# Kernel optimization log

Hardware: AMD Instinct MI355X
Metric: run time of the kernel (lower is better)

## Reference

```python
import jax, jax.numpy as jnp
import numpy as np

N, IN_DIM, HID, M, T, E, A, OUT = 10000, 256, 256, 8, 3, 160000, 2000, 10
LN_EPS = 1e-5


def _layernorm(x, g, b):
    mu = x.mean(-1, keepdims=True)
    var = ((x - mu) ** 2).mean(-1, keepdims=True)
    return (x - mu) * jax.lax.rsqrt(var + LN_EPS) * g + b


def _gcn_conv(x, w, b, src, dst, n):
    # PyG GCNConv: x' = D^{-1/2}(A+I)D^{-1/2} (x W) + b, deg counted on dst with self-loops
    xw = x @ w  # [n, out]
    loops = jnp.arange(n, dtype=src.dtype)
    s = jnp.concatenate([src, loops])
    d = jnp.concatenate([dst, loops])
    deg = jax.ops.segment_sum(jnp.ones(d.shape[0], xw.dtype), d, num_segments=n)
    dinv = jax.lax.rsqrt(jnp.maximum(deg, 1.0))
    norm = dinv[s] * dinv[d]
    out = jax.ops.segment_sum(xw[s] * norm[:, None], d, num_segments=n)
    return out + b


def setup_inputs() -> dict:
    key = jax.random.key(0)
    ks = jax.random.split(key, 26)
    g = lambda i, shape: (jax.random.normal(ks[i], shape, jnp.float32) * 0.02)
    return {
        "edge_index_t": jax.random.randint(ks[0], (T, 2, E), 0, N),
        "node_t": jax.random.randint(ks[1], (T, A), 0, N),
        "m": M,
        "emb": g(2, (N, IN_DIM)),
        "gcn_w1": g(3, (IN_DIM, HID)), "gcn_b1": jnp.zeros((HID,), jnp.float32),
        "gcn_w2": g(4, (HID, HID)), "gcn_b2": jnp.zeros((HID,), jnp.float32),
        "ln1_g": jnp.ones((HID,), jnp.float32), "ln1_b": jnp.zeros((HID,), jnp.float32),
        "tok_w1": g(5, (M, M)), "tok_b1": jnp.zeros((M,), jnp.float32),
        "tok_w2": g(6, (M, M)), "tok_b2": jnp.zeros((M,), jnp.float32),
        "ln2_g": jnp.ones((HID,), jnp.float32), "ln2_b": jnp.zeros((HID,), jnp.float32),
        "ch_w1": g(7, (HID, HID)), "ch_b1": jnp.zeros((HID,), jnp.float32),
        "ch_w2": g(8, (HID, HID)), "ch_b2": jnp.zeros((HID,), jnp.float32),
        "pred_w": g(9, (HID, HID)), "pred_b": jnp.zeros((HID,), jnp.float32),
        "cls1_w": g(10, (HID, HID)), "cls1_b": jnp.zeros((HID,), jnp.float32),
        "cls2_w": g(11, (HID, OUT)), "cls2_b": jnp.zeros((OUT,), jnp.float32),
    }


def reference(edge_index_t, node_t, m, emb,
              gcn_w1, gcn_b1, gcn_w2, gcn_b2,
              ln1_g, ln1_b, tok_w1, tok_b1, tok_w2, tok_b2,
              ln2_g, ln2_b, ch_w1, ch_b1, ch_w2, ch_b2,
              pred_w, pred_b, cls1_w, cls1_b, cls2_w, cls2_b):
    n = emb.shape[0]

    def mixer(xm):  # [n, m, hid]
        y = _layernorm(xm, ln1_g, ln1_b)
        # token MLP over the m axis (transpose(1,2) in torch)
        y = jnp.einsum('nmh,mk->nkh', y, tok_w1) + tok_b1[None, :, None]
        y = jax.nn.gelu(y, approximate=False)
        y = jnp.einsum('nmh,mk->nkh', y, tok_w2) + tok_b2[None, :, None]
        x = xm + y
        z = _layernorm(x, ln2_g, ln2_b)
        z = jax.nn.gelu(z @ ch_w1 + ch_b1, approximate=False) @ ch_w2 + ch_b2
        return x + z

    def step(x_m, inp):
        src, dst, nid = inp
        # forecast from current window (before this step's graph update)
        x_new = mixer(x_m).mean(axis=1)  # discrete FinalProcessLayer: mean over tokens
        # 2-layer GCN on the (shared) initial embeddings
        x = _gcn_conv(emb, gcn_w1, gcn_b1, src, dst, n)
        x = jax.nn.relu(x)
        x = _gcn_conv(x, gcn_w2, gcn_b2, src, dst, n)
        # boolean-mask scatter: zero rows of nodes listed in node_t[i]
        x = x.at[nid].set(0.0)
        x_m = jnp.concatenate([x_m[:, 1:, :], x[:, None, :]], axis=1)
        return x_m, x_new

    x_m0 = jnp.zeros((n, m, HID), emb.dtype)
    _, v = jax.lax.scan(step, x_m0, (edge_index_t[:, 0], edge_index_t[:, 1], node_t))
    # InvariantPredictor over all T timesteps at once: v [T, n, hid]
    h = jnp.tanh(v @ pred_w + pred_b)
    y_hat = jax.nn.relu((h @ cls1_w + cls1_b) @ cls2_w + cls2_b)
    return h, y_hat
```

## Files before the change

kernel.cpp:

```cpp
#include <hip/hip_runtime.h>
#include <math.h>

#define NN 10000
#define HIDD 256
#define MTOK 8
#define TT 3
#define EE 160000
#define AA 2000
#define OUTD 10
#define LNEPS 1e-5f

typedef unsigned short u16;
typedef __attribute__((ext_vector_type(8))) __bf16 bf16x8;
typedef __attribute__((ext_vector_type(4))) float f32x4;

__device__ __forceinline__ float gelu_f(float x) {
    return 0.5f * x * (1.f + erff(x * 0.7071067811865475f));
}
__device__ __forceinline__ u16 f2bf(float x) {
    unsigned u = __builtin_bit_cast(unsigned, x);
    return (u16)((u + 0x7FFFu + ((u >> 16) & 1u)) >> 16);
}
__device__ __forceinline__ float bf2f(u16 b) {
    return __builtin_bit_cast(float, (unsigned)b << 16);
}
__device__ __forceinline__ void gload16(const void* g, void* l) {
    __builtin_amdgcn_global_load_lds(
        (const __attribute__((address_space(1))) unsigned int*)g,
        (__attribute__((address_space(3))) unsigned int*)l, 16, 0, 0);
}

__global__ void count_kernel(const int* __restrict__ edge, int* __restrict__ cnt) {
    int g = blockIdx.y;
    const int* dst = edge + (size_t)g * 2 * EE + EE;
    int e = blockIdx.x * 256 + threadIdx.x;
    if (e < EE) atomicAdd(&cnt[g * NN + dst[e]], 1);
}

__global__ __launch_bounds__(1024) void scan_kernel(const int* __restrict__ cnt_all,
        int* __restrict__ rowstart_all, int* __restrict__ cursor_all, float* __restrict__ dinv_all) {
    int g = blockIdx.x;
    const int* cnt = cnt_all + (size_t)g * NN;
    int* rowstart = rowstart_all + (size_t)g * NN;
    int* cursor = cursor_all + (size_t)g * NN;
    float* dinv = dinv_all + (size_t)g * NN;
    __shared__ int wsum[16];
    int tid = threadIdx.x, lane = tid & 63, wid = tid >> 6;
    int carry = 0;
    for (int base = 0; base < NN; base += 1024) {
        int i = base + tid;
        int v = (i < NN) ? cnt[i] : 0;
        int s = v;
        #pragma unroll
        for (int o = 1; o < 64; o <<= 1) {
            int t = __shfl_up(s, o, 64);
            if (lane >= o) s += t;
        }
        if (lane == 63) wsum[wid] = s;
        __syncthreads();
        if (wid == 0) {
            int ws = (lane < 16) ? wsum[lane] : 0;
            #pragma unroll
            for (int o = 1; o < 16; o <<= 1) {
                int t = __shfl_up(ws, o, 64);
                if (lane >= o) ws += t;
            }
            if (lane < 16) wsum[lane] = ws;
        }
        __syncthreads();
        int woff = (wid > 0) ? wsum[wid - 1] : 0;
        int tot = wsum[15];
        if (i < NN) {
            int excl = carry + s + woff - v;
            rowstart[i] = excl;
            cursor[i] = excl;
            dinv[i] = rsqrtf((float)(v + 1));
        }
        carry += tot;
        __syncthreads();
    }
}

__global__ void fill_kernel(const int* __restrict__ edge, int* __restrict__ cursor, int* __restrict__ esrc) {
    int g = blockIdx.y;
    const int* src = edge + (size_t)g * 2 * EE;
    const int* dst = src + EE;
    int e = blockIdx.x * 256 + threadIdx.x;
    if (e < EE) {
        int d = dst[e];
        int idx = atomicAdd(&cursor[g * NN + d], 1);
        esrc[(size_t)g * EE + idx] = src[e];
    }
}

template<int RELU, int WF32, int WSPLIT>
__global__ __launch_bounds__(256) void gcn_agg(const float* __restrict__ xw, size_t xw_goff,
        const int* __restrict__ esrc_all, const int* __restrict__ rowstart_all,
        const int* __restrict__ cnt_all, const float* __restrict__ dinv_all,
        const float* __restrict__ bias, float* __restrict__ out,
        u16* __restrict__ ohi, u16* __restrict__ olo) {
    int g = blockIdx.y;
    const float* xwg = xw + (size_t)g * xw_goff;
    const int* esrc = esrc_all + (size_t)g * EE;
    const int* rowstart = rowstart_all + (size_t)g * NN;
    const int* cntp = cnt_all + (size_t)g * NN;
    const float* dinv = dinv_all + (size_t)g * NN;
    int wave = threadIdx.x >> 6, lane = threadIdx.x & 63;
    int d = blockIdx.x * 4 + wave;
    if (d >= NN) return;
    int start = rowstart[d];
    int len = cntp[d];
    float dd = dinv[d];
    int h = lane * 4;
    float4 a = *(const float4*)&xwg[(size_t)d * HIDD + h];
    float4 acc;
    acc.x = a.x * dd; acc.y = a.y * dd; acc.z = a.z * dd; acc.w = a.w * dd;
    for (int i = 0; i < len; i++) {
        int s = esrc[start + i];
        float ds = dinv[s];
        float4 b = *(const float4*)&xwg[(size_t)s * HIDD + h];
        acc.x = fmaf(b.x, ds, acc.x);
        acc.y = fmaf(b.y, ds, acc.y);
        acc.z = fmaf(b.z, ds, acc.z);
        acc.w = fmaf(b.w, ds, acc.w);
    }
    float o0 = acc.x * dd + bias[h + 0];
    float o1 = acc.y * dd + bias[h + 1];
    float o2 = acc.z * dd + bias[h + 2];
    float o3 = acc.w * dd + bias[h + 3];
    if (RELU) {
        o0 = fmaxf(o0, 0.f); o1 = fmaxf(o1, 0.f); o2 = fmaxf(o2, 0.f); o3 = fmaxf(o3, 0.f);
    }
    size_t obase = (size_t)g * NN * HIDD + (size_t)d * HIDD + h;
    if (WF32) {
        float4 o; o.x = o0; o.y = o1; o.z = o2; o.w = o3;
        *(float4*)&out[obase] = o;
    }
    if (WSPLIT) {
        ushort4 hv, lv;
        u16 h0 = f2bf(o0), h1 = f2bf(o1), h2 = f2bf(o2), h3 = f2bf(o3);
        hv.x = h0; hv.y = h1; hv.z = h2; hv.w = h3;
        lv.x = f2bf(o0 - bf2f(h0)); lv.y = f2bf(o1 - bf2f(h1));
        lv.z = f2bf(o2 - bf2f(h2)); lv.w = f2bf(o3 - bf2f(h3));
        *(ushort4*)&ohi[obase] = hv;
        *(ushort4*)&olo[obase] = lv;
    }
}

__global__ void mask_kernel(const int* __restrict__ node_t, float* __restrict__ xs) {
    int g = blockIdx.y;
    int node = node_t[(size_t)g * AA + blockIdx.x];
    xs[(size_t)g * NN * HIDD + (size_t)node * HIDD + threadIdx.x] = 0.f;
}

__global__ void split_kernel(const float* __restrict__ x, u16* __restrict__ hi, u16* __restrict__ lo, int n) {
    int i = blockIdx.x * 256 + threadIdx.x;
    if (i < n) {
        float v = x[i];
        u16 h = f2bf(v);
        hi[i] = h;
        lo[i] = f2bf(v - bf2f(h));
    }
}

__global__ void wsplit_all(const float* __restrict__ w0, const float* __restrict__ w1,
        const float* __restrict__ w2, const float* __restrict__ w3,
        const float* __restrict__ w4, const float* __restrict__ w5, u16* __restrict__ bt) {
    const float* W[6] = { w0, w1, w2, w3, w4, w5 };
    const float* Wm = W[blockIdx.y];
    u16* Bt = bt + (size_t)blockIdx.y * 256 * 768;
    int c = blockIdx.x, k = threadIdx.x;
    float x = Wm[k * 256 + c];
    u16 hi = f2bf(x), lo = f2bf(x - bf2f(hi));
    Bt[c * 768 + k] = hi;
    Bt[c * 768 + 256 + k] = hi;
    Bt[c * 768 + 512 + k] = lo;
}

template<int ACT, int WF32, int WSPLIT, int EPI>
__global__ __launch_bounds__(256) void gemm_split(
        const u16* __restrict__ Ahi, const u16* __restrict__ Alo,
        const u16* __restrict__ Bt, const float* __restrict__ bias,
        float* __restrict__ outf, u16* __restrict__ ohi, u16* __restrict__ olo,
        const float* __restrict__ xsum, int R) {
    __shared__ __align__(16) u16 ldsA[2][128 * 64];
    __shared__ __align__(16) u16 ldsB[2][128 * 64];
    int tid = threadIdx.x;
    int lane = tid & 63, w = tid >> 6;
    int nwg = gridDim.x, orig = blockIdx.x;
    int xcd = orig & 7, i8 = orig >> 3;
    int q = nwg >> 3, r = nwg & 7;
    int bid = (xcd < r ? xcd * (q + 1) : r * (q + 1) + (xcd - r) * q) + i8;
    int rowbase = (bid >> 1) * 128;
    int cb = bid & 1;
    int wrow = (w >> 1) * 64, wcol = (w & 1) * 64;
    f32x4 acc[4][4];
    #pragma unroll
    for (int i = 0; i < 4; i++)
        #pragma unroll
        for (int j = 0; j < 4; j++) acc[i][j] = f32x4{0.f, 0.f, 0.f, 0.f};

    constexpr int KCH[12]  = {0,4,1,5,2,6,3,7,8,9,10,11};
    constexpr int BNEW[12] = {1,0,1,0,1,0,1,0,1,1,1,1};
    constexpr int BBUF[12] = {0,0,1,1,0,0,1,1,0,1,0,1};

    auto stageA = [&](int buf, int c) {
        const u16* Aseg = (c >= 4 && c < 8) ? Alo : Ahi;
        int koff = (c & 3) * 64;
        #pragma unroll
        for (int i = 0; i < 4; i++) {
            int j = i * 256 + tid;
            int rr = j >> 3, sl = j & 7;
            int grow = rowbase + rr; if (grow > R - 1) grow = R - 1;
            const u16* gp = Aseg + (size_t)grow * 256 + koff + ((sl ^ (rr & 7)) << 3);
            gload16(gp, &ldsA[buf][(i * 256 + (tid & 192)) << 3]);
        }
    };
    auto stageB = [&](int buf, int c) {
        #pragma unroll
        for (int i = 0; i < 4; i++) {
            int j = i * 256 + tid;
            int rr = j >> 3, sl = j & 7;
            const u16* gp = Bt + (size_t)(cb * 128 + rr) * 768 + c * 64 + ((sl ^ (rr & 7)) << 3);
            gload16(gp, &ldsB[buf][(i * 256 + (tid & 192)) << 3]);
        }
    };

    stageA(0, KCH[0]);
    stageB(0, KCH[0]);
    #pragma unroll
    for (int c = 0; c < 12; c++) {
        int cur = c & 1;
        if (c < 11) {
            stageA(cur ^ 1, KCH[c + 1]);
            if (BNEW[c + 1]) {
                stageB(BBUF[c + 1], KCH[c + 1]);
                asm volatile("s_waitcnt vmcnt(8)" ::: "memory");
            } else {
                asm volatile("s_waitcnt vmcnt(4)" ::: "memory");
            }
        } else {
            asm volatile("s_waitcnt vmcnt(0)" ::: "memory");
        }
        __builtin_amdgcn_s_barrier();
        __builtin_amdgcn_sched_barrier(0);
        __builtin_amdgcn_s_setprio(1);
        #pragma unroll
        for (int ks = 0; ks < 2; ks++) {
            bf16x8 a[4], b[4];
            #pragma unroll
            for (int rf = 0; rf < 4; rf++) {
                int rr = wrow + rf * 16 + (lane & 15);
                int slot = (lane >> 4) + ks * 4;
                a[rf] = *(const bf16x8*)&ldsA[cur][(rr << 6) + ((slot ^ (rr & 7)) << 3)];
            }
            #pragma unroll
            for (int cf = 0; cf < 4; cf++) {
                int cc = wcol + cf * 16 + (lane & 15);
                int slot = (lane >> 4) + ks * 4;
                b[cf] = *(const bf16x8*)&ldsB[BBUF[c]][(cc << 6) + ((slot ^ (cc & 7)) << 3)];
            }
            #pragma unroll
            for (int rf = 0; rf < 4; rf++)
                #pragma unroll
                for (int cf = 0; cf < 4; cf++)
                    acc[rf][cf] = __builtin_amdgcn_mfma_f32_16x16x32_bf16(a[rf], b[cf], acc[rf][cf], 0, 0, 0);
        }
        __builtin_amdgcn_s_setprio(0);
        __builtin_amdgcn_sched_barrier(0);
        __builtin_amdgcn_s_barrier();
    }
    #pragma unroll
    for (int rf = 0; rf < 4; rf++) {
        #pragma unroll
        for (int cf = 0; cf < 4; cf++) {
            int col = cb * 128 + wcol + cf * 16 + (lane & 15);
            float bv = bias[col];
            f32x4 v = acc[rf][cf];
            if (EPI == 1) {
                float s = 0.f;
                #pragma unroll
                for (int r2 = 0; r2 < 4; r2++) s += gelu_f(v[r2] + bv);
                float o = __shfl_xor(s, 16, 64);
                float nodesum = s + o;
                if (((lane >> 4) & 1) == 0) {
                    int node = ((rowbase + wrow + rf * 16) >> 3) + ((lane >> 4) >> 1);
                    u16 hi = f2bf(nodesum), lo = f2bf(nodesum - bf2f(hi));
                    ohi[(size_t)node * 256 + col] = hi;
                    olo[(size_t)node * 256 + col] = lo;
                }
            } else if (EPI == 2) {
                int row0 = rowbase + wrow + rf * 16 + ((lane >> 4) << 2);
                #pragma unroll
                for (int r2 = 0; r2 < 4; r2++) {
                    int row = row0 + r2;
                    if (row < R) {
                        float val = (xsum[(size_t)row * 256 + col] + v[r2] + 8.f * bv) * 0.125f;
                        u16 hi = f2bf(val), lo = f2bf(val - bf2f(hi));
                        ohi[(size_t)row * 256 + col] = hi;
                        olo[(size_t)row * 256 + col] = lo;
                    }
                }
            } else {
                int row0 = rowbase + wrow + rf * 16 + ((lane >> 4) << 2);
                #pragma unroll
                for (int r2 = 0; r2 < 4; r2++) {
                    int row = row0 + r2;
                    if (row < R) {
                        float val = v[r2] + bv;
                        if (ACT == 1) val = gelu_f(val);
                        if (ACT == 2) val = tanhf(val);
                        if (WF32) outf[(size_t)row * 256 + col] = val;
                        if (WSPLIT) {
                            u16 hi = f2bf(val), lo = f2bf(val - bf2f(hi));
                            ohi[(size_t)row * 256 + col] = hi;
                            olo[(size_t)row * 256 + col] = lo;
                        }
                    }
                }
            }
        }
    }
}

__global__ __launch_bounds__(256) void mixer_front(
        const float* __restrict__ xs, int nodebase,
        const float* __restrict__ ln1_g, const float* __restrict__ ln1_b,
        const float* __restrict__ tw1, const float* __restrict__ tb1,
        const float* __restrict__ tw2, const float* __restrict__ tb2,
        const float* __restrict__ ln2_g, const float* __restrict__ ln2_b,
        u16* __restrict__ z_hi, u16* __restrict__ z_lo, float* __restrict__ xsum_out) {
    int nv = nodebase + blockIdx.x;
    int step = nv >= NN ? 1 : 0;
    int n = nv - step * NN;
    const float* p1 = xs + ((size_t)step * NN + n) * HIDD;
    const float* p2 = step ? xs + (size_t)n * HIDD : nullptr;
    int tid = threadIdx.x;
    int wave = tid >> 6, lane = tid & 63;
    __shared__ __align__(16) float sx[MTOK][HIDD];
    __shared__ float stw1[64], stw2[64], stb1[8], stb2[8];
    __shared__ float red[MTOK][2];
    if (tid < 64) { stw1[tid] = tw1[tid]; stw2[tid] = tw2[tid]; }
    if (tid < 8)  { stb1[tid] = tb1[tid]; stb2[tid] = tb2[tid]; }
    #pragma unroll
    for (int m = 0; m < MTOK; m++) {
        const float* src = (m == MTOK - 1) ? p1 : (m == MTOK - 2) ? p2 : nullptr;
        sx[m][tid] = src ? src[tid] : 0.f;
    }
    __syncthreads();
    float g1v = ln1_g[tid], b1v = ln1_b[tid];
    #pragma unroll
    for (int rep = 0; rep < 2; rep++) {
        int m = wave + rep * 4;
        float x0 = sx[m][lane], x1 = sx[m][lane + 64], x2 = sx[m][lane + 128], x3 = sx[m][lane + 192];
        float s = x0 + x1 + x2 + x3;
        float ss = x0 * x0 + x1 * x1 + x2 * x2 + x3 * x3;
        for (int off = 32; off > 0; off >>= 1) { s += __shfl_down(s, off, 64); ss += __shfl_down(ss, off, 64); }
        if (lane == 0) {
            float mu = s * (1.f / HIDD);
            float var = ss * (1.f / HIDD) - mu * mu;
            red[m][0] = mu;
            red[m][1] = rsqrtf(var + LNEPS);
        }
    }
    __syncthreads();
    float ty[MTOK];
    #pragma unroll
    for (int m = 0; m < MTOK; m++) ty[m] = (sx[m][tid] - red[m][0]) * red[m][1] * g1v + b1v;
    float u[MTOK];
    #pragma unroll
    for (int k = 0; k < MTOK; k++) {
        float a = stb1[k];
        #pragma unroll
        for (int m = 0; m < MTOK; m++) a = fmaf(ty[m], stw1[m * MTOK + k], a);
        u[k] = gelu_f(a);
    }
    #pragma unroll
    for (int k = 0; k < MTOK; k++) {
        float a = stb2[k];
        #pragma unroll
        for (int m = 0; m < MTOK; m++) a = fmaf(u[m], stw2[m * MTOK + k], a);
        sx[k][tid] += a;
    }
    __syncthreads();
    float xsm = 0.f;
    #pragma unroll
    for (int m = 0; m < MTOK; m++) xsm += sx[m][tid];
    xsum_out[(size_t)nv * HIDD + tid] = xsm;
    float g2v = ln2_g[tid], b2v = ln2_b[tid];
    #pragma unroll
    for (int rep = 0; rep < 2; rep++) {
        int m = wave + rep * 4;
        float x0 = sx[m][lane], x1 = sx[m][lane + 64], x2 = sx[m][lane + 128], x3 = sx[m][lane + 192];
        float s = x0 + x1 + x2 + x3;
        float ss = x0 * x0 + x1 * x1 + x2 * x2 + x3 * x3;
        for (int off = 32; off > 0; off >>= 1) { s += __shfl_down(s, off, 64); ss += __shfl_down(ss, off, 64); }
        if (lane == 0) {
            float mu = s * (1.f / HIDD);
            float var = ss * (1.f / HIDD) - mu * mu;
            red[m][0] = mu;
            red[m][1] = rsqrtf(var + LNEPS);
        }
    }
    __syncthreads();
    #pragma unroll
    for (int m = 0; m < MTOK; m++) {
        float z = (sx[m][tid] - red[m][0]) * red[m][1] * g2v + b2v;
        u16 hi = f2bf(z), lo = f2bf(z - bf2f(hi));
        size_t idx = ((size_t)blockIdx.x * MTOK + m) * HIDD + tid;
        z_hi[idx] = hi;
        z_lo[idx] = lo;
    }
}

__global__ __launch_bounds__(256) void mixer_kernel(
        const float* __restrict__ ln1_g, const float* __restrict__ ln1_b,
        const float* __restrict__ tw1, const float* __restrict__ tb1,
        const float* __restrict__ tw2, const float* __restrict__ tb2,
        const float* __restrict__ ln2_g, const float* __restrict__ ln2_b,
        const float* __restrict__ cw1, const float* __restrict__ cb1,
        const float* __restrict__ cw2, const float* __restrict__ cb2,
        float* __restrict__ vout) {
    int tid = threadIdx.x;
    __shared__ __align__(16) float sx[MTOK][HIDD];
    __shared__ __align__(16) float sy[MTOK][HIDD];
    __shared__ float stw1[64], stw2[64], stb1[8], stb2[8];
    if (tid < 64) { stw1[tid] = tw1[tid]; stw2[tid] = tw2[tid]; }
    if (tid < 8)  { stb1[tid] = tb1[tid]; stb2[tid] = tb2[tid]; }
    __syncthreads();
    float b1v = ln1_b[tid];
    float ty[MTOK];
    #pragma unroll
    for (int m = 0; m < MTOK; m++) ty[m] = b1v;
    float u[MTOK];
    #pragma unroll
    for (int k = 0; k < MTOK; k++) {
        float a = stb1[k];
        #pragma unroll
        for (int m = 0; m < MTOK; m++) a = fmaf(ty[m], stw1[m * MTOK + k], a);
        u[k] = gelu_f(a);
    }
    #pragma unroll
    for (int k = 0; k < MTOK; k++) {
        float a = stb2[k];
        #pragma unroll
        for (int m = 0; m < MTOK; m++) a = fmaf(u[m], stw2[m * MTOK + k], a);
        sx[k][tid] = a;
    }
    __syncthreads();
    __shared__ float red[MTOK][2];
    int wave = tid >> 6, lane = tid & 63;
    float g2v = ln2_g[tid], b2v = ln2_b[tid];
    #pragma unroll
    for (int rep = 0; rep < 2; rep++) {
        int m = wave + rep * 4;
        float x0 = sx[m][lane], x1 = sx[m][lane + 64], x2 = sx[m][lane + 128], x3 = sx[m][lane + 192];
        float s = x0 + x1 + x2 + x3;
        float ss = x0 * x0 + x1 * x1 + x2 * x2 + x3 * x3;
        for (int off = 32; off > 0; off >>= 1) { s += __shfl_down(s, off, 64); ss += __shfl_down(ss, off, 64); }
        if (lane == 0) {
            float mu = s * (1.f / HIDD);
            float var = ss * (1.f / HIDD) - mu * mu;
            red[m][0] = mu;
            red[m][1] = rsqrtf(var + LNEPS);
        }
    }
    __syncthreads();
    #pragma unroll
    for (int m = 0; m < MTOK; m++) sy[m][tid] = (sx[m][tid] - red[m][0]) * red[m][1] * g2v + b2v;
    __syncthreads();
    float acc[MTOK];
    #pragma unroll
    for (int m = 0; m < MTOK; m++) acc[m] = 0.f;
    for (int h = 0; h < HIDD; h += 4) {
        float w0 = cw1[(h + 0) * HIDD + tid];
        float w1 = cw1[(h + 1) * HIDD + tid];
        float w2 = cw1[(h + 2) * HIDD + tid];
        float w3 = cw1[(h + 3) * HIDD + tid];
        #pragma unroll
        for (int m = 0; m < MTOK; m++) {
            const float4 a = *(const float4*)&sy[m][h];
            acc[m] = fmaf(a.x, w0, acc[m]);
            acc[m] = fmaf(a.y, w1, acc[m]);
            acc[m] = fmaf(a.z, w2, acc[m]);
            acc[m] = fmaf(a.w, w3, acc[m]);
        }
    }
    __syncthreads();
    float cb1v = cb1[tid];
    #pragma unroll
    for (int m = 0; m < MTOK; m++) sy[m][tid] = gelu_f(acc[m] + cb1v);
    __syncthreads();
    float acc2[MTOK];
    #pragma unroll
    for (int m = 0; m < MTOK; m++) acc2[m] = 0.f;
    for (int h = 0; h < HIDD; h += 4) {
        float w0 = cw2[(h + 0) * HIDD + tid];
        float w1 = cw2[(h + 1) * HIDD + tid];
        float w2 = cw2[(h + 2) * HIDD + tid];
        float w3 = cw2[(h + 3) * HIDD + tid];
        #pragma unroll
        for (int m = 0; m < MTOK; m++) {
            const float4 a = *(const float4*)&sy[m][h];
            acc2[m] = fmaf(a.x, w0, acc2[m]);
            acc2[m] = fmaf(a.y, w1, acc2[m]);
            acc2[m] = fmaf(a.z, w2, acc2[m]);
            acc2[m] = fmaf(a.w, w3, acc2[m]);
        }
    }
    float cb2v = cb2[tid];
    float ssum = 0.f;
    #pragma unroll
    for (int m = 0; m < MTOK; m++) ssum += sx[m][tid] + acc2[m] + cb2v;
    vout[tid] = ssum * (1.f / MTOK);
}

__global__ __launch_bounds__(256) void t0_head(const float* __restrict__ v0row,
        const float* __restrict__ pred_w, const float* __restrict__ pred_b,
        const float* __restrict__ cls1_w, const float* __restrict__ cls1_b,
        const float* __restrict__ cls2_w, const float* __restrict__ cls2_b,
        float* __restrict__ h0row, float* __restrict__ y0row) {
    __shared__ float s[HIDD], s2[HIDD];
    int tid = threadIdx.x;
    s[tid] = v0row[tid];
    __syncthreads();
    float a = 0.f;
    for (int k = 0; k < HIDD; k++) a = fmaf(s[k], pred_w[k * HIDD + tid], a);
    float h = tanhf(a + pred_b[tid]);
    h0row[tid] = h;
    s2[tid] = h;
    __syncthreads();
    a = 0.f;
    for (int k = 0; k < HIDD; k++) a = fmaf(s2[k], cls1_w[k * HIDD + tid], a);
    float g = a + cls1_b[tid];
    __syncthreads();
    s[tid] = g;
    __syncthreads();
    if (tid < OUTD) {
        float y = 0.f;
        for (int k = 0; k < HIDD; k++) y = fmaf(s[k], cls2_w[k * OUTD + tid], y);
        y0row[tid] = fmaxf(y + cls2_b[tid], 0.f);
    }
}

__global__ void bcast_both(const float* __restrict__ h0row, const float* __restrict__ y0row,
        float* __restrict__ hout, float* __restrict__ yout) {
    int n = blockIdx.x, tid = threadIdx.x;
    hout[(size_t)n * HIDD + tid] = h0row[tid];
    if (tid < OUTD) yout[(size_t)n * OUTD + tid] = y0row[tid];
}

__global__ __launch_bounds__(256) void cls2_kernel(const float* __restrict__ g1, const float* __restrict__ wm,
        const float* __restrict__ b, float* __restrict__ out, int rows) {
    __shared__ float sw[HIDD][12];
    int tid = threadIdx.x;
    for (int i = tid; i < HIDD * OUTD; i += 256) sw[i / OUTD][i % OUTD] = wm[i];
    __syncthreads();
    int rl = tid >> 4, kk = tid & 15;
    int r = blockIdx.x * 16 + rl;
    if (r < rows && kk < OUTD) {
        float acc = 0.f;
        const float* grow = g1 + (size_t)r * HIDD;
        for (int h = 0; h < HIDD; h++) acc = fmaf(grow[h], sw[h][kk], acc);
        out[(size_t)r * OUTD + kk] = fmaxf(acc + b[kk], 0.f);
    }
}

extern "C" void kernel_launch(void* const* d_in, const int* in_sizes, int n_in,
                              void* d_out, int out_size, void* d_ws, size_t ws_size,
                              hipStream_t stream) {
    const int* edge    = (const int*)d_in[0];
    const int* node_t  = (const int*)d_in[1];
    const float* emb   = (const float*)d_in[3];
    const float* gcn_w1 = (const float*)d_in[4];
    const float* gcn_b1 = (const float*)d_in[5];
    const float* gcn_w2 = (const float*)d_in[6];
    const float* gcn_b2 = (const float*)d_in[7];
    const float* ln1_g = (const float*)d_in[8];
    const float* ln1_b = (const float*)d_in[9];
    const float* tw1   = (const float*)d_in[10];
    const float* tb1   = (const float*)d_in[11];
    const float* tw2   = (const float*)d_in[12];
    const float* tb2   = (const float*)d_in[13];
    const float* ln2_g = (const float*)d_in[14];
    const float* ln2_b = (const float*)d_in[15];
    const float* cw1   = (const float*)d_in[16];
    const float* cb1   = (const float*)d_in[17];
    const float* cw2   = (const float*)d_in[18];
    const float* cb2   = (const float*)d_in[19];
    const float* pred_w = (const float*)d_in[20];
    const float* pred_b = (const float*)d_in[21];
    const float* cls1_w = (const float*)d_in[22];
    const float* cls1_b = (const float*)d_in[23];
    const float* cls2_w = (const float*)d_in[24];
    const float* cls2_b = (const float*)d_in[25];

    const size_t NH = (size_t)NN * HIDD;
    char* wsb = (char*)d_ws;
    size_t off = 0;
    auto alloc = [&](size_t bytes) { char* p = wsb + off; off = (off + bytes + 255) & ~(size_t)255; return p; };
    float* xs   = (float*)alloc(2 * NH * 4);
    u16* v_hi   = (u16*)alloc(2 * NH * 2);
    u16* v_lo   = (u16*)alloc(2 * NH * 2);
    u16* h_hi   = (u16*)alloc(2 * NH * 2);
    u16* h_lo   = (u16*)alloc(2 * NH * 2);
    float* xw2  = (float*)alloc(2 * NH * 4);
    float* xsum = (float*)alloc(2 * NH * 4);
    u16* Bt_all = (u16*)alloc((size_t)6 * 256 * 768 * 2);
    u16* Bt_cw1  = Bt_all;
    u16* Bt_cw2  = Bt_all + 1 * 256 * 768;
    u16* Bt_pred = Bt_all + 2 * 256 * 768;
    u16* Bt_cls1 = Bt_all + 3 * 256 * 768;
    u16* Bt_gw1  = Bt_all + 4 * 256 * 768;
    u16* Bt_gw2  = Bt_all + 5 * 256 * 768;
    float* dinv  = (float*)alloc(2 * NN * 4);
    float* zeros = (float*)alloc(HIDD * 4);
    float* v0row = (float*)alloc(HIDD * 4);
    float* h0row = (float*)alloc(HIDD * 4);
    float* y0row = (float*)alloc(16 * 4);
    int* cnt    = (int*)alloc(2 * NN * 4);
    int* rowst  = (int*)alloc(2 * NN * 4);
    int* cursor = (int*)alloc(2 * NN * 4);
    int* esrc   = (int*)alloc((size_t)2 * EE * 4);
    float* xw    = (float*)h_hi;
    u16*  emb_hi = h_lo;
    u16*  emb_lo = h_lo + NH;
    u16*  agg_hi = v_hi;
    u16*  agg_lo = v_lo;
    u16*  s2_hi  = (u16*)xw2;
    u16*  s2_lo  = (u16*)xw2 + 2 * NH;
    float* g1    = xw2;
    size_t remain = (ws_size > off + 4096) ? (ws_size - off - 4096) : 0;
    int CHN = (int)(remain / 8192);
    if (CHN > 2 * NN) CHN = 2 * NN;
    CHN &= ~15;
    if (CHN < 16) CHN = 16;
    const size_t ZE = (size_t)CHN * MTOK * HIDD;
    u16* z_hi  = (u16*)alloc(ZE * 2);
    u16* z_lo  = (u16*)alloc(ZE * 2);

    float* h_out = (float*)d_out;
    float* y_out = h_out + (size_t)TT * NH;

    hipMemsetAsync(zeros, 0, HIDD * sizeof(float), stream);
    wsplit_all<<<dim3(256, 6), 256, 0, stream>>>(cw1, cw2, pred_w, cls1_w, gcn_w1, gcn_w2, Bt_all);
    split_kernel<<<(NN * HIDD + 255) / 256, 256, 0, stream>>>(emb, emb_hi, emb_lo, NN * HIDD);
    gemm_split<0, 1, 0, 0><<<2 * ((NN + 127) / 128), 256, 0, stream>>>(
        emb_hi, emb_lo, Bt_gw1, zeros, xw, nullptr, nullptr, nullptr, NN);

    mixer_kernel<<<1, 256, 0, stream>>>(ln1_g, ln1_b, tw1, tb1, tw2, tb2,
        ln2_g, ln2_b, cw1, cb1, cw2, cb2, v0row);
    t0_head<<<1, 256, 0, stream>>>(v0row, pred_w, pred_b, cls1_w, cls1_b,
        cls2_w, cls2_b, h0row, y0row);
    bcast_both<<<NN, 256, 0, stream>>>(h0row, y0row, h_out, y_out);

    hipMemsetAsync(cnt, 0, 2 * NN * sizeof(int), stream);
    count_kernel<<<dim3((EE + 255) / 256, 2), 256, 0, stream>>>(edge, cnt);
    scan_kernel<<<2, 1024, 0, stream>>>(cnt, rowst, cursor, dinv);
    fill_kernel<<<dim3((EE + 255) / 256, 2), 256, 0, stream>>>(edge, cursor, esrc);
    gcn_agg<1, 0, 1><<<dim3((NN + 3) / 4, 2), 256, 0, stream>>>(xw, 0,
        esrc, rowst, cnt, dinv, gcn_b1, nullptr, agg_hi, agg_lo);
    gemm_split<0, 1, 0, 0><<<2 * ((2 * NN + 127) / 128), 256, 0, stream>>>(
        agg_hi, agg_lo, Bt_gw2, zeros, xw2, nullptr, nullptr, nullptr, 2 * NN);
    gcn_agg<0, 1, 0><<<dim3((NN + 3) / 4, 2), 256, 0, stream>>>(xw2, NH,
        esrc, rowst, cnt, dinv, gcn_b2, xs, nullptr, nullptr);
    mask_kernel<<<dim3(AA, 2), 256, 0, stream>>>(node_t, xs);

    for (int nb = 0; nb < 2 * NN; nb += CHN) {
        int nodes = 2 * NN - nb < CHN ? 2 * NN - nb : CHN;
        int R = nodes * MTOK;
        int rb = (R + 127) / 128;
        mixer_front<<<nodes, 256, 0, stream>>>(xs, nb,
            ln1_g, ln1_b, tw1, tb1, tw2, tb2, ln2_g, ln2_b, z_hi, z_lo, xsum);
        gemm_split<1, 0, 0, 1><<<2 * rb, 256, 0, stream>>>(
            z_hi, z_lo, Bt_cw1, cb1, nullptr,
            s2_hi + (size_t)nb * HIDD, s2_lo + (size_t)nb * HIDD, nullptr, R);
    }
    gemm_split<0, 0, 0, 2><<<2 * ((2 * NN + 127) / 128), 256, 0, stream>>>(
        s2_hi, s2_lo, Bt_cw2, cb2, nullptr, v_hi, v_lo, xsum, 2 * NN);
    gemm_split<2, 1, 1, 0><<<2 * ((2 * NN + 127) / 128), 256, 0, stream>>>(
        v_hi, v_lo, Bt_pred, pred_b,
        h_out + NH, h_hi, h_lo, nullptr, 2 * NN);
    gemm_split<0, 1, 0, 0><<<2 * ((2 * NN + 127) / 128), 256, 0, stream>>>(
        h_hi, h_lo, Bt_cls1, cls1_b, g1, nullptr, nullptr, nullptr, 2 * NN);
    cls2_kernel<<<(2 * NN + 15) / 16, 256, 0, stream>>>(g1, cls2_w, cls2_b, y_out + (size_t)NN * OUTD, 2 * NN);
}
```

Before: 583.9 us.

## Fuse token-mixer front and cw1 GEMM into one kernel keeping z in LDS

Merges the mixer_front kernel (LayerNorms plus the token MLP) with the following cw1 GEMM. Each block now processes 4 nodes (32 rows) and keeps the bf16 hi/lo z tile in shared memory, while streaming the cw1 weight through double-buffered LDS. The chunked global z_hi/z_lo buffer and its write/read round trip disappear, along with the multi-launch loop. In exchange, each block redoes the full B-matrix load for only 32 rows, which raises weight traffic and leaves small, possibly underutilised MFMA tiles.

```diff
diff --git a/kernel.cpp b/kernel.cpp
--- a/kernel.cpp
+++ b/kernel.cpp
@@ -277,19 +277,7 @@
             int col = cb * 128 + wcol + cf * 16 + (lane & 15);
             float bv = bias[col];
             f32x4 v = acc[rf][cf];
-            if (EPI == 1) {
-                float s = 0.f;
-                #pragma unroll
-                for (int r2 = 0; r2 < 4; r2++) s += gelu_f(v[r2] + bv);
-                float o = __shfl_xor(s, 16, 64);
-                float nodesum = s + o;
-                if (((lane >> 4) & 1) == 0) {
-                    int node = ((rowbase + wrow + rf * 16) >> 3) + ((lane >> 4) >> 1);
-                    u16 hi = f2bf(nodesum), lo = f2bf(nodesum - bf2f(hi));
-                    ohi[(size_t)node * 256 + col] = hi;
-                    olo[(size_t)node * 256 + col] = lo;
-                }
-            } else if (EPI == 2) {
+            if (EPI == 2) {
                 int row0 = rowbase + wrow + rf * 16 + ((lane >> 4) << 2);
                 #pragma unroll
                 for (int r2 = 0; r2 < 4; r2++) {
@@ -323,93 +311,182 @@
     }
 }
 
-__global__ __launch_bounds__(256) void mixer_front(
-        const float* __restrict__ xs, int nodebase,
+__global__ __launch_bounds__(256, 2) void mixer_cw1(
+        const float* __restrict__ xs, const u16* __restrict__ Bt, const float* __restrict__ cb1,
         const float* __restrict__ ln1_g, const float* __restrict__ ln1_b,
         const float* __restrict__ tw1, const float* __restrict__ tb1,
         const float* __restrict__ tw2, const float* __restrict__ tb2,
         const float* __restrict__ ln2_g, const float* __restrict__ ln2_b,
-        u16* __restrict__ z_hi, u16* __restrict__ z_lo, float* __restrict__ xsum_out) {
-    int nv = nodebase + blockIdx.x;
-    int step = nv >= NN ? 1 : 0;
-    int n = nv - step * NN;
-    const float* p1 = xs + ((size_t)step * NN + n) * HIDD;
-    const float* p2 = step ? xs + (size_t)n * HIDD : nullptr;
-    int tid = threadIdx.x;
-    int wave = tid >> 6, lane = tid & 63;
+        float* __restrict__ xsum_out, u16* __restrict__ s2_hi, u16* __restrict__ s2_lo) {
     __shared__ __align__(16) float sx[MTOK][HIDD];
+    __shared__ __align__(16) u16 zhi[32 * 256];
+    __shared__ __align__(16) u16 zlo[32 * 256];
+    __shared__ __align__(16) u16 ldsB[2][128 * 64];
     __shared__ float stw1[64], stw2[64], stb1[8], stb2[8];
     __shared__ float red[MTOK][2];
+    int tid = threadIdx.x, lane = tid & 63, w = tid >> 6;
+
+    auto stageB = [&](int buf, int chunk, int ch) {
+        #pragma unroll
+        for (int i = 0; i < 4; i++) {
+            int j = i * 256 + tid;
+            int rr = j >> 3, sl = j & 7;
+            const u16* gp = Bt + (size_t)(ch * 128 + rr) * 768 + chunk * 64 + ((sl ^ (rr & 7)) << 3);
+            gload16(gp, &ldsB[buf][(i * 256 + (tid & 192)) << 3]);
+        }
+    };
+
     if (tid < 64) { stw1[tid] = tw1[tid]; stw2[tid] = tw2[tid]; }
     if (tid < 8)  { stb1[tid] = tb1[tid]; stb2[tid] = tb2[tid]; }
-    #pragma unroll
-    for (int m = 0; m < MTOK; m++) {
-        const float* src = (m == MTOK - 1) ? p1 : (m == MTOK - 2) ? p2 : nullptr;
-        sx[m][tid] = src ? src[tid] : 0.f;
-    }
-    __syncthreads();
+    stageB(0, 0, 0);
+
     float g1v = ln1_g[tid], b1v = ln1_b[tid];
-    #pragma unroll
-    for (int rep = 0; rep < 2; rep++) {
-        int m = wave + rep * 4;
-        float x0 = sx[m][lane], x1 = sx[m][lane + 64], x2 = sx[m][lane + 128], x3 = sx[m][lane + 192];
-        float s = x0 + x1 + x2 + x3;
-        float ss = x0 * x0 + x1 * x1 + x2 * x2 + x3 * x3;
-        for (int off = 32; off > 0; off >>= 1) { s += __shfl_down(s, off, 64); ss += __shfl_down(ss, off, 64); }
-        if (lane == 0) {
-            float mu = s * (1.f / HIDD);
-            float var = ss * (1.f / HIDD) - mu * mu;
-            red[m][0] = mu;
-            red[m][1] = rsqrtf(var + LNEPS);
-        }
-    }
-    __syncthreads();
-    float ty[MTOK];
-    #pragma unroll
-    for (int m = 0; m < MTOK; m++) ty[m] = (sx[m][tid] - red[m][0]) * red[m][1] * g1v + b1v;
-    float u[MTOK];
-    #pragma unroll
-    for (int k = 0; k < MTOK; k++) {
-        float a = stb1[k];
-        #pragma unroll
-        for (int m = 0; m < MTOK; m++) a = fmaf(ty[m], stw1[m * MTOK + k], a);
-        u[k] = gelu_f(a);
-    }
-    #pragma unroll
-    for (int k = 0; k < MTOK; k++) {
-        float a = stb2[k];
-        #pragma unroll
-        for (int m = 0; m < MTOK; m++) a = fmaf(u[m], stw2[m * MTOK + k], a);
-        sx[k][tid] += a;
-    }
-    __syncthreads();
-    float xsm = 0.f;
-    #pragma unroll
-    for (int m = 0; m < MTOK; m++) xsm += sx[m][tid];
-    xsum_out[(size_t)nv * HIDD + tid] = xsm;
     float g2v = ln2_g[tid], b2v = ln2_b[tid];
-    #pragma unroll
-    for (int rep = 0; rep < 2; rep++) {
-        int m = wave + rep * 4;
-        float x0 = sx[m][lane], x1 = sx[m][lane + 64], x2 = sx[m][lane + 128], x3 = sx[m][lane + 192];
-        float s = x0 + x1 + x2 + x3;
-        float ss = x0 * x0 + x1 * x1 + x2 * x2 + x3 * x3;
-        for (int off = 32; off > 0; off >>= 1) { s += __shfl_down(s, off, 64); ss += __shfl_down(ss, off, 64); }
-        if (lane == 0) {
-            float mu = s * (1.f / HIDD);
-            float var = ss * (1.f / HIDD) - mu * mu;
-            red[m][0] = mu;
-            red[m][1] = rsqrtf(var + LNEPS);
-        }
-    }
-    __syncthreads();
-    #pragma unroll
-    for (int m = 0; m < MTOK; m++) {
-        float z = (sx[m][tid] - red[m][0]) * red[m][1] * g2v + b2v;
-        u16 hi = f2bf(z), lo = f2bf(z - bf2f(hi));
-        size_t idx = ((size_t)blockIdx.x * MTOK + m) * HIDD + tid;
-        z_hi[idx] = hi;
-        z_lo[idx] = lo;
+
+    for (int i = 0; i < 4; i++) {
+        int nv = blockIdx.x * 4 + i;
+        int step = nv >= NN ? 1 : 0;
+        int n = nv - step * NN;
+        const float* p1 = xs + ((size_t)step * NN + n) * HIDD;
+        const float* p2 = step ? xs + (size_t)n * HIDD : nullptr;
+        __syncthreads();
+        #pragma unroll
+        for (int m = 0; m < MTOK; m++) {
+            const float* src = (m == MTOK - 1) ? p1 : (m == MTOK - 2) ? p2 : nullptr;
+            sx[m][tid] = src ? src[tid] : 0.f;
+        }
+        __syncthreads();
+        #pragma unroll
+        for (int rep = 0; rep < 2; rep++) {
+            int m = w + rep * 4;
+            float x0 = sx[m][lane], x1 = sx[m][lane + 64], x2 = sx[m][lane + 128], x3 = sx[m][lane + 192];
+            float s = x0 + x1 + x2 + x3;
+            float ss = x0 * x0 + x1 * x1 + x2 * x2 + x3 * x3;
+            for (int off = 32; off > 0; off >>= 1) { s += __shfl_down(s, off, 64); ss += __shfl_down(ss, off, 64); }
+            if (lane == 0) {
+                float mu = s * (1.f / HIDD);
+                float var = ss * (1.f / HIDD) - mu * mu;
+                red[m][0] = mu;
+                red[m][1] = rsqrtf(var + LNEPS);
+            }
+        }
+        __syncthreads();
+        float ty[MTOK];
+        #pragma unroll
+        for (int m = 0; m < MTOK; m++) ty[m] = (sx[m][tid] - red[m][0]) * red[m][1] * g1v + b1v;
+        float u[MTOK];
+        #pragma unroll
+        for (int k = 0; k < MTOK; k++) {
+            float a = stb1[k];
+            #pragma unroll
+            for (int m = 0; m < MTOK; m++) a = fmaf(ty[m], stw1[m * MTOK + k], a);
+            u[k] = gelu_f(a);
+        }
+        #pragma unroll
+        for (int k = 0; k < MTOK; k++) {
+            float a = stb2[k];
+            #pragma unroll
+            for (int m = 0; m < MTOK; m++) a = fmaf(u[m], stw2[m * MTOK + k], a);
+            sx[k][tid] += a;
+        }
+        __syncthreads();
+        float xsm = 0.f;
+        #pragma unroll
+        for (int m = 0; m < MTOK; m++) xsm += sx[m][tid];
+        xsum_out[(size_t)nv * HIDD + tid] = xsm;
+        #pragma unroll
+        for (int rep = 0; rep < 2; rep++) {
+            int m = w + rep * 4;
+            float x0 = sx[m][lane], x1 = sx[m][lane + 64], x2 = sx[m][lane + 128], x3 = sx[m][lane + 192];
+            float s = x0 + x1 + x2 + x3;
+            float ss = x0 * x0 + x1 * x1 + x2 * x2 + x3 * x3;
+            for (int off = 32; off > 0; off >>= 1) { s += __shfl_down(s, off, 64); ss += __shfl_down(ss, off, 64); }
+            if (lane == 0) {
+                float mu = s * (1.f / HIDD);
+                float var = ss * (1.f / HIDD) - mu * mu;
+                red[m][0] = mu;
+                red[m][1] = rsqrtf(var + LNEPS);
+            }
+        }
+        __syncthreads();
+        #pragma unroll
+        for (int m = 0; m < MTOK; m++) {
+            float z = (sx[m][tid] - red[m][0]) * red[m][1] * g2v + b2v;
+            u16 hi = f2bf(z), lo = f2bf(z - bf2f(hi));
+            int row = i * 8 + m;
+            int kidx = (tid & 0xC0) | (((((tid >> 3) & 7) ^ (row & 7))) << 3) | (tid & 7);
+            zhi[row * 256 + kidx] = hi;
+            zlo[row * 256 + kidx] = lo;
+        }
+    }
+
+    for (int ch = 0; ch < 2; ch++) {
+        f32x4 acc[2][2];
+        #pragma unroll
+        for (int a0 = 0; a0 < 2; a0++)
+            #pragma unroll
+            for (int b0 = 0; b0 < 2; b0++) acc[a0][b0] = f32x4{0.f, 0.f, 0.f, 0.f};
+        if (ch == 1) stageB(0, 0, 1);
+        #pragma unroll
+        for (int c = 0; c < 12; c++) {
+            int cur = c & 1;
+            if (c < 11) {
+                stageB(cur ^ 1, c + 1, ch);
+                asm volatile("s_waitcnt vmcnt(4)" ::: "memory");
+            } else {
+                asm volatile("s_waitcnt vmcnt(0)" ::: "memory");
+            }
+            __builtin_amdgcn_s_barrier();
+            __builtin_amdgcn_sched_barrier(0);
+            __builtin_amdgcn_s_setprio(1);
+            const u16* Z = (c >= 4 && c < 8) ? zlo : zhi;
+            int koff = (c & 3) * 64;
+            #pragma unroll
+            for (int ks = 0; ks < 2; ks++) {
+                bf16x8 a[2], b[2];
+                #pragma unroll
+                for (int rf = 0; rf < 2; rf++) {
+                    int rr = rf * 16 + (lane & 15);
+                    int slot = (lane >> 4) + ks * 4;
+                    a[rf] = *(const bf16x8*)&Z[rr * 256 + koff + ((slot ^ (rr & 7)) << 3)];
+                }
+                #pragma unroll
+                for (int cf = 0; cf < 2; cf++) {
+                    int cc = w * 32 + cf * 16 + (lane & 15);
+                    int slot = (lane >> 4) + ks * 4;
+                    b[cf] = *(const bf16x8*)&ldsB[cur][(cc << 6) + ((slot ^ (cc & 7)) << 3)];
+                }
+                #pragma unroll
+                for (int rf = 0; rf < 2; rf++)
+                    #pragma unroll
+                    for (int cf = 0; cf < 2; cf++)
+                        acc[rf][cf] = __builtin_amdgcn_mfma_f32_16x16x32_bf16(a[rf], b[cf], acc[rf][cf], 0, 0, 0);
+            }
+            __builtin_amdgcn_s_setprio(0);
+            __builtin_amdgcn_sched_barrier(0);
+            __builtin_amdgcn_s_barrier();
+        }
+        #pragma unroll
+        for (int rf = 0; rf < 2; rf++) {
+            #pragma unroll
+            for (int cf = 0; cf < 2; cf++) {
+                int col = ch * 128 + w * 32 + cf * 16 + (lane & 15);
+                float bv = cb1[col];
+                f32x4 v = acc[rf][cf];
+                float s = 0.f;
+                #pragma unroll
+                for (int r2 = 0; r2 < 4; r2++) s += gelu_f(v[r2] + bv);
+                float o = __shfl_xor(s, 16, 64);
+                float nodesum = s + o;
+                if (((lane >> 4) & 1) == 0) {
+                    int nloc = rf * 2 + ((lane >> 4) >> 1);
+                    int nv = blockIdx.x * 4 + nloc;
+                    u16 hi = f2bf(nodesum), lo = f2bf(nodesum - bf2f(hi));
+                    s2_hi[(size_t)nv * 256 + col] = hi;
+                    s2_lo[(size_t)nv * 256 + col] = lo;
+                }
+            }
+        }
     }
 }
 
@@ -630,14 +707,6 @@
     u16*  s2_hi  = (u16*)xw2;
     u16*  s2_lo  = (u16*)xw2 + 2 * NH;
     float* g1    = xw2;
-    size_t remain = (ws_size > off + 4096) ? (ws_size - off - 4096) : 0;
-    int CHN = (int)(remain / 8192);
-    if (CHN > 2 * NN) CHN = 2 * NN;
-    CHN &= ~15;
-    if (CHN < 16) CHN = 16;
-    const size_t ZE = (size_t)CHN * MTOK * HIDD;
-    u16* z_hi  = (u16*)alloc(ZE * 2);
-    u16* z_lo  = (u16*)alloc(ZE * 2);
 
     float* h_out = (float*)d_out;
     float* y_out = h_out + (size_t)TT * NH;
@@ -666,16 +735,9 @@
         esrc, rowst, cnt, dinv, gcn_b2, xs, nullptr, nullptr);
     mask_kernel<<<dim3(AA, 2), 256, 0, stream>>>(node_t, xs);
 
-    for (int nb = 0; nb < 2 * NN; nb += CHN) {
-        int nodes = 2 * NN - nb < CHN ? 2 * NN - nb : CHN;
-        int R = nodes * MTOK;
-        int rb = (R + 127) / 128;
-        mixer_front<<<nodes, 256, 0, stream>>>(xs, nb,
-            ln1_g, ln1_b, tw1, tb1, tw2, tb2, ln2_g, ln2_b, z_hi, z_lo, xsum);
-        gemm_split<1, 0, 0, 1><<<2 * rb, 256, 0, stream>>>(
-            z_hi, z_lo, Bt_cw1, cb1, nullptr,
-            s2_hi + (size_t)nb * HIDD, s2_lo + (size_t)nb * HIDD, nullptr, R);
-    }
+    mixer_cw1<<<2 * NN / 4, 256, 0, stream>>>(xs, Bt_cw1, cb1,
+        ln1_g, ln1_b, tw1, tb1, tw2, tb2, ln2_g, ln2_b, xsum, s2_hi, s2_lo);
+
     gemm_split<0, 0, 0, 2><<<2 * ((2 * NN + 127) / 128), 256, 0, stream>>>(
         s2_hi, s2_lo, Bt_cw2, cb2, nullptr, v_hi, v_lo, xsum, 2 * NN);
     gemm_split<2, 1, 1, 0><<<2 * ((2 * NN + 127) / 128), 256, 0, stream>>>(
```

Measured after the change: 653.7 us. 1.12x slower.
